# Performance work log

Hardware: AMD Instinct MI355X
Metric: run time of the kernel (lower is better)

The kernel has to match this reference:

```python
import jax, jax.numpy as jnp
import numpy as np

B, C, H, W = 16, 256, 32, 32
K = 3          # kernel size
KK = K * K     # matrix_batch = 9 kernel positions
N = 256        # out_channels = n (power of 2, nstack = 1)


def setup_inputs() -> dict:
    key = jax.random.key(0)
    k1, k2, k3, k4 = jax.random.split(key, 4)
    s = 1.0 / np.sqrt(2.0)  # repo's 'regular' param init scale
    return {
        "x": jax.random.normal(k1, (B, C, H, W), jnp.float32),
        "twiddle1": jax.random.normal(k2, (KK, N - 1, 2, 2), jnp.float32) * s,
        "twiddle2": jax.random.normal(k3, (KK, N - 1, 2, 2), jnp.float32) * s,
        "bias": jax.random.normal(k4, (KK, N), jnp.float32) * 0.01,
    }


def _butterfly_tied(twiddle, x, increasing):
    """Tied-weight butterfly multiply.
    twiddle: (s, n-1, 2, 2); x: (b, s, n). At stride st, twiddle[:, st-1:2*st-1]
    (length st) is shared across the n/(2*st) blocks (matches butterfly_mult_torch).
    """
    b, s, n = x.shape
    m = n.bit_length() - 1  # log2(n)
    strides = [1 << i for i in range(m)]
    if not increasing:
        strides = strides[::-1]
    for st in strides:
        t = twiddle[:, st - 1:2 * st - 1]            # (s, st, 2, 2)
        xr = x.reshape(b, s, n // (2 * st), 2, st)   # (b, s, g, 2, st)
        # out[b,s,g,i,l] = sum_k t[s,l,i,k] * xr[b,s,g,k,l]
        x = jnp.einsum('slik,bsgkl->bsgil', t, xr).reshape(b, s, n)
    return x


def reference(x, twiddle1, twiddle2, bias):
    b, c, h, w = x.shape
    # im2col / F.unfold with kernel 3, pad 1, stride 1 -> (b, c, 9, h*w),
    # kernel positions in row-major order (matches torch unfold layout).
    xp = jnp.pad(x, ((0, 0), (0, 0), (1, 1), (1, 1)))
    patches = jnp.stack(
        [xp[:, :, i:i + h, j:j + w] for i in range(K) for j in range(K)], axis=2
    )  # (b, c, 9, h, w)
    inp = patches.reshape(b, c, KK, h * w).transpose(0, 3, 2, 1)
    inp = inp.reshape(b * h * w, KK, c)  # (batch*h*w, 9, c)
    # BB^T: B^T (decreasing stride) then B (increasing stride), bias on last.
    y = _butterfly_tied(twiddle1, inp, increasing=False)
    y = _butterfly_tied(twiddle2, y, increasing=True) + bias  # bias: (9, N)
    out = y.mean(axis=1)  # average over the 9 kernel positions -> (b*h*w, N)
    return out.reshape(b, h * w, N).transpose(0, 2, 1).reshape(b, N, h, w)
```

## Files before the change

### kernel.cpp

```cpp
#include <hip/hip_runtime.h>
#include <hip/hip_bf16.h>

typedef __attribute__((ext_vector_type(8))) short short8;
typedef __attribute__((ext_vector_type(4))) float float4v;
typedef __attribute__((ext_vector_type(16))) float float16v;

#define XT_BYTES (16*32*34*34*8*2)
#define WG_BYTES (9*4*4*8*64*8*2)

__global__ __launch_bounds__(256) void k_prep(const float* __restrict__ x,
                                              const float* __restrict__ tw1,
                                              const float* __restrict__ tw2,
                                              const float* __restrict__ bias,
                                              __hip_bfloat16* __restrict__ xTg,
                                              __hip_bfloat16* __restrict__ Wg,
                                              float* __restrict__ biasout) {
  __shared__ __align__(16) char smem[256 * 33 * 4];
  int blk = blockIdx.x;
  int tid = threadIdx.x;

  if (blk < 512) {
    float* tile = (float*)smem;
    char* xTB = (char*)xTg;
    int h = blk & 31, b = blk >> 5;
    {
      int w4 = (tid & 7) * 4, c0 = tid >> 3;
#pragma unroll
      for (int j = 0; j < 8; ++j) {
        int ci = c0 + 32 * j;
        float4 v = *(const float4*)&x[((b * 256 + ci) * 32 + h) * 32 + w4];
        *(float4*)&tile[ci * 33 + w4] = v;
      }
    }
    __syncthreads();
    {
      int g0 = tid >> 5, w = tid & 31;
#pragma unroll
      for (int gi = 0; gi < 4; ++gi) {
        int g = gi * 8 + g0;
        union { short8 s; __hip_bfloat16 hv[8]; } pk;
#pragma unroll
        for (int cc = 0; cc < 8; ++cc)
          pk.hv[cc] = __float2bfloat16(tile[(g * 8 + cc) * 33 + w]);
        *(short8*)(xTB + ((((b * 32 + g) * 34 + h + 1) * 34) + (w + 1)) * 16) = pk.s;
      }
    }
    if (h < 2) {
      uint4 z4 = {0u, 0u, 0u, 0u};
      int edge = h * 33;
      for (int i = tid; i < 32 * 34; i += 256) {
        int g = i / 34, w = i - g * 34;
        *(uint4*)(xTB + ((((b * 32 + g) * 34 + edge) * 34) + w) * 16) = z4;
      }
      for (int i = tid; i < 32 * 32; i += 256) {
        int g = i >> 5, hh = 1 + (i & 31);
        *(uint4*)(xTB + ((((b * 32 + g) * 34 + hh) * 34) + edge) * 16) = z4;
      }
    }
    return;
  }

  int wblk = blk - 512;
  if (wblk == 144) {
    if (tid < 256) {
      float a = 0.f;
#pragma unroll
      for (int s = 0; s < 9; ++s) a += bias[s * 256 + tid];
      biasout[tid] = a * (1.f / 9.f);
    }
    return;
  }
  float* mat = (float*)smem;
  float* tws = (float*)(smem + 17408);
  int sidx = wblk >> 4;
  int colbase = (wblk & 15) * 16;

  for (int i = tid; i < 255 * 4; i += 256) {
    tws[i]           = tw1[sidx * 255 * 4 + i];
    tws[255 * 4 + i] = tw2[sidx * 255 * 4 + i];
  }
  {
    int r = tid;
#pragma unroll
    for (int c = 0; c < 16; ++c) mat[r * 17 + c] = (r == colbase + c) ? 1.f : 0.f;
  }

  int c  = tid & 15;
  int pg = tid >> 4;
  for (int ph = 0; ph < 2; ++ph) {
    for (int si = 0; si < 8; ++si) {
      int lg = ph ? si : (7 - si);
      int st = 1 << lg;
      __syncthreads();
      float x0[8], x1[8], t0[8], t1[8], t2[8], t3[8];
#pragma unroll
      for (int i = 0; i < 8; ++i) {
        int qp = pg * 8 + i;
        int li = qp & (st - 1);
        int gi = qp >> lg;
        int p0 = (gi << (lg + 1)) | li;
        int p1 = p0 + st;
        float4 tv = *(const float4*)&tws[(ph * 255 + st - 1 + li) * 4];
        t0[i] = tv.x; t1[i] = tv.y; t2[i] = tv.z; t3[i] = tv.w;
        x0[i] = mat[p0 * 17 + c];
        x1[i] = mat[p1 * 17 + c];
      }
#pragma unroll
      for (int i = 0; i < 8; ++i) {
        int qp = pg * 8 + i;
        int li = qp & (st - 1);
        int gi = qp >> lg;
        int p0 = (gi << (lg + 1)) | li;
        int p1 = p0 + st;
        mat[p0 * 17 + c] = t0[i] * x0[i] + t1[i] * x1[i];
        mat[p1 * 17 + c] = t2[i] * x0[i] + t3[i] * x1[i];
      }
    }
  }
  __syncthreads();

  for (int idx = tid; idx < 256 * 16; idx += 256) {
    int r = idx >> 4, cc = idx & 15;
    int cg = colbase + cc;
    int pr = cg >> 6, g = (cg >> 3) & 7, c8 = cg & 7;
    int nq = r >> 6, nl = r & 63;
    int o = ((((sidx * 4 + pr) * 4 + nq) * 8 + g) * 64 + nl) * 8 + c8;
    Wg[o] = __float2bfloat16(mat[r * 17 + cc] * (1.f / 9.f));
  }
}

__global__ __launch_bounds__(256, 4) void k_gemm(const __hip_bfloat16* __restrict__ xTg,
                                                 const __hip_bfloat16* __restrict__ Wg,
                                                 const float* __restrict__ biasout,
                                                 float* __restrict__ out) {
  __shared__ __align__(64) char lds[16384];
  const char* WgB = (const char*)Wg;
  const char* xTB = (const char*)xTg;

  int blk  = blockIdx.x;
  int rest = blk >> 3;
  int b    = 2 * (blk & 7) + (rest >> 6);
  int r2   = rest & 63;
  int nq   = r2 & 3;
  int pt   = r2 >> 2;
  int h0   = pt * 2;

  int tid  = threadIdx.x;
  int lane = tid & 63;
  int wk   = tid >> 6;
  int half = lane >> 5;
  int l31  = lane & 31;

  float16v acc[2][2];
#pragma unroll
  for (int mt = 0; mt < 2; ++mt)
#pragma unroll
    for (int p2 = 0; p2 < 2; ++p2)
#pragma unroll
      for (int e = 0; e < 16; ++e) acc[mt][p2][e] = 0.f;

  int aoff = ((2 * wk + half) * 64 + l31) * 16;
  int bbase = ((((b * 32 + 2 * wk + half) * 34 + h0) * 34) + l31) * 16;

#pragma unroll 2
  for (int p = 0; p < 4; ++p) {
    const char* Bp = xTB + bbase + p * (8 * 34 * 34) * 16;
    const char* Ap = WgB + (p * 4 + nq) * 8192;
#pragma unroll
    for (int si = 0; si < 3; ++si) {
#pragma unroll
      for (int sj = 0; sj < 3; ++sj) {
        const char* Aslab = Ap + (si * 3 + sj) * (16 * 8192);
        short8 a0 = *(const short8*)(Aslab + aoff);
        short8 a1 = *(const short8*)(Aslab + aoff + 32 * 16);
        const char* Bq = Bp + (si * 34 + sj) * 16;
        short8 b0 = *(const short8*)(Bq);
        short8 b1 = *(const short8*)(Bq + 34 * 16);
        acc[0][0] = __builtin_amdgcn_mfma_f32_32x32x16_bf16(a0, b0, acc[0][0], 0, 0, 0);
        acc[0][1] = __builtin_amdgcn_mfma_f32_32x32x16_bf16(a0, b1, acc[0][1], 0, 0, 0);
        acc[1][0] = __builtin_amdgcn_mfma_f32_32x32x16_bf16(a1, b0, acc[1][0], 0, 0, 0);
        acc[1][1] = __builtin_amdgcn_mfma_f32_32x32x16_bf16(a1, b1, acc[1][1], 0, 0, 0);
      }
    }
  }

  auto st16 = [&](int slot, const float16v& v) {
    char* base = lds + slot * 4096 + lane * 16;
    *(float4v*)(base)        = (float4v){v[0],  v[1],  v[2],  v[3]};
    *(float4v*)(base + 1024) = (float4v){v[4],  v[5],  v[6],  v[7]};
    *(float4v*)(base + 2048) = (float4v){v[8],  v[9],  v[10], v[11]};
    *(float4v*)(base + 3072) = (float4v){v[12], v[13], v[14], v[15]};
  };
  auto ld16add = [&](int slot, float16v& v) {
    const char* base = lds + slot * 4096 + lane * 16;
    float4v t0 = *(const float4v*)(base);
    float4v t1 = *(const float4v*)(base + 1024);
    float4v t2 = *(const float4v*)(base + 2048);
    float4v t3 = *(const float4v*)(base + 3072);
    v[0] += t0[0]; v[1] += t0[1]; v[2]  += t0[2]; v[3]  += t0[3];
    v[4] += t1[0]; v[5] += t1[1]; v[6]  += t1[2]; v[7]  += t1[3];
    v[8] += t2[0]; v[9] += t2[1]; v[10] += t2[2]; v[11] += t2[3];
    v[12] += t3[0]; v[13] += t3[1]; v[14] += t3[2]; v[15] += t3[3];
  };

  __syncthreads();
  if (wk >= 2) {
#pragma unroll
    for (int p2 = 0; p2 < 2; ++p2) st16((wk - 2) * 2 + p2, acc[0][p2]);
  }
  __syncthreads();
  if (wk < 2) {
#pragma unroll
    for (int p2 = 0; p2 < 2; ++p2) ld16add(wk * 2 + p2, acc[0][p2]);
  }
  __syncthreads();
  if (wk >= 2) {
#pragma unroll
    for (int p2 = 0; p2 < 2; ++p2) st16((wk - 2) * 2 + p2, acc[1][p2]);
  }
  __syncthreads();
  if (wk < 2) {
#pragma unroll
    for (int p2 = 0; p2 < 2; ++p2) ld16add(wk * 2 + p2, acc[1][p2]);
  }
  __syncthreads();
  if (wk == 1) {
#pragma unroll
    for (int p2 = 0; p2 < 2; ++p2) { st16(p2, acc[0][p2]); st16(2 + p2, acc[1][p2]); }
  }
  __syncthreads();
  if (wk == 0) {
#pragma unroll
    for (int p2 = 0; p2 < 2; ++p2) { ld16add(p2, acc[0][p2]); ld16add(2 + p2, acc[1][p2]); }
#pragma unroll
    for (int mt = 0; mt < 2; ++mt) {
#pragma unroll
      for (int reg = 0; reg < 16; ++reg) {
        int n = nq * 64 + mt * 32 + (reg & 3) + 8 * (reg >> 2) + 4 * half;
        float bv = biasout[n];
#pragma unroll
        for (int p2 = 0; p2 < 2; ++p2)
          out[((b * 256 + n) * 32 + h0 + p2) * 32 + l31] = acc[mt][p2][reg] + bv;
      }
    }
  }
}

extern "C" void kernel_launch(void* const* d_in, const int* in_sizes, int n_in,
                              void* d_out, int out_size, void* d_ws, size_t ws_size,
                              hipStream_t stream) {
  const float* x    = (const float*)d_in[0];
  const float* tw1  = (const float*)d_in[1];
  const float* tw2  = (const float*)d_in[2];
  const float* bias = (const float*)d_in[3];
  float* out = (float*)d_out;

  char* ws = (char*)d_ws;
  __hip_bfloat16* xTg = (__hip_bfloat16*)ws;
  __hip_bfloat16* Wg  = (__hip_bfloat16*)(ws + XT_BYTES);
  float* biasout      = (float*)(ws + XT_BYTES + WG_BYTES);

  k_prep<<<657, 256, 0, stream>>>(x, tw1, tw2, bias, xTg, Wg, biasout);
  k_gemm<<<1024, 256, 0, stream>>>(xTg, Wg, biasout, out);
}
```

Baseline: 108.4 us.

## Software-pipeline GEMM global loads with six-deep register ring and inline asm

Replaces the compiler-scheduled load/MFMA loop in k_gemm with a fully unrolled software pipeline. Loads of A and B fragments for six future steps are held in a register ring, issued via inline asm global_load_dwordx4 and gated by explicit s_waitcnt vmcnt counts, with sched barriers pinning the order. The aim is to hide global memory latency behind MFMA work. Occupancy hint drops from 4 to 2 blocks per SIMD to make room for the extra live registers, which may reduce latency hiding across waves.

```diff
diff --git a/kernel.cpp b/kernel.cpp
--- a/kernel.cpp
+++ b/kernel.cpp
@@ -129,7 +129,30 @@
   }
 }
 
-__global__ __launch_bounds__(256, 4) void k_gemm(const __hip_bfloat16* __restrict__ xTg,
+
+#define ISSUE(SL, P, S, SI, SJ)                                               \
+  { const char* ap_ = pA + (P)*32768 + (S)*131072;                            \
+    const char* bp_ = pB + (P)*147968 + (SI)*544 + (SJ)*16;                   \
+    asm volatile("global_load_dwordx4 %0, %2, off\n\t"                        \
+                 "global_load_dwordx4 %1, %2, off offset:512"                 \
+      : "=&v"(ra[SL][0]), "=&v"(ra[SL][1]) : "v"(ap_));                       \
+    asm volatile("global_load_dwordx4 %0, %2, off\n\t"                        \
+                 "global_load_dwordx4 %1, %2, off offset:544"                 \
+      : "=&v"(rb[SL][0]), "=&v"(rb[SL][1]) : "v"(bp_)); }
+
+#define WAITB_(N) asm volatile("s_waitcnt vmcnt(" #N ")" ::: "memory")
+#define WAITB(N) WAITB_(N); __builtin_amdgcn_sched_barrier(0)
+
+#define MM4(SL)                                                               \
+  acc[0][0] = __builtin_amdgcn_mfma_f32_32x32x16_bf16(ra[SL][0], rb[SL][0], acc[0][0], 0, 0, 0); \
+  acc[0][1] = __builtin_amdgcn_mfma_f32_32x32x16_bf16(ra[SL][0], rb[SL][1], acc[0][1], 0, 0, 0); \
+  acc[1][0] = __builtin_amdgcn_mfma_f32_32x32x16_bf16(ra[SL][1], rb[SL][0], acc[1][0], 0, 0, 0); \
+  acc[1][1] = __builtin_amdgcn_mfma_f32_32x32x16_bf16(ra[SL][1], rb[SL][1], acc[1][1], 0, 0, 0);
+
+#define BODY(SL, JP, JS, JSI, JSJ) { WAITB(20); MM4(SL); ISSUE(SL, JP, JS, JSI, JSJ); }
+#define BODYT(SL, N)               { WAITB(N);  MM4(SL); }
+
+__global__ __launch_bounds__(256, 2) void k_gemm(const __hip_bfloat16* __restrict__ xTg,
                                                  const __hip_bfloat16* __restrict__ Wg,
                                                  const float* __restrict__ biasout,
                                                  float* __restrict__ out) {
@@ -160,29 +183,27 @@
       for (int e = 0; e < 16; ++e) acc[mt][p2][e] = 0.f;
 
   int aoff = ((2 * wk + half) * 64 + l31) * 16;
+  const char* pA = WgB + nq * 8192 + aoff;
   int bbase = ((((b * 32 + 2 * wk + half) * 34 + h0) * 34) + l31) * 16;
-
-#pragma unroll 2
-  for (int p = 0; p < 4; ++p) {
-    const char* Bp = xTB + bbase + p * (8 * 34 * 34) * 16;
-    const char* Ap = WgB + (p * 4 + nq) * 8192;
-#pragma unroll
-    for (int si = 0; si < 3; ++si) {
-#pragma unroll
-      for (int sj = 0; sj < 3; ++sj) {
-        const char* Aslab = Ap + (si * 3 + sj) * (16 * 8192);
-        short8 a0 = *(const short8*)(Aslab + aoff);
-        short8 a1 = *(const short8*)(Aslab + aoff + 32 * 16);
-        const char* Bq = Bp + (si * 34 + sj) * 16;
-        short8 b0 = *(const short8*)(Bq);
-        short8 b1 = *(const short8*)(Bq + 34 * 16);
-        acc[0][0] = __builtin_amdgcn_mfma_f32_32x32x16_bf16(a0, b0, acc[0][0], 0, 0, 0);
-        acc[0][1] = __builtin_amdgcn_mfma_f32_32x32x16_bf16(a0, b1, acc[0][1], 0, 0, 0);
-        acc[1][0] = __builtin_amdgcn_mfma_f32_32x32x16_bf16(a1, b0, acc[1][0], 0, 0, 0);
-        acc[1][1] = __builtin_amdgcn_mfma_f32_32x32x16_bf16(a1, b1, acc[1][1], 0, 0, 0);
-      }
-    }
-  }
+  const char* pB = xTB + bbase;
+
+  short8 ra[6][2];
+  short8 rb[6][2];
+
+  ISSUE(0, 0,0,0,0) ISSUE(1, 0,1,0,1) ISSUE(2, 0,2,0,2)
+  ISSUE(3, 0,3,1,0) ISSUE(4, 0,4,1,1) ISSUE(5, 0,5,1,2)
+
+  BODY(0, 0,6,2,0) BODY(1, 0,7,2,1) BODY(2, 0,8,2,2)
+  BODY(3, 1,0,0,0) BODY(4, 1,1,0,1) BODY(5, 1,2,0,2)
+  BODY(0, 1,3,1,0) BODY(1, 1,4,1,1) BODY(2, 1,5,1,2)
+  BODY(3, 1,6,2,0) BODY(4, 1,7,2,1) BODY(5, 1,8,2,2)
+  BODY(0, 2,0,0,0) BODY(1, 2,1,0,1) BODY(2, 2,2,0,2)
+  BODY(3, 2,3,1,0) BODY(4, 2,4,1,1) BODY(5, 2,5,1,2)
+  BODY(0, 2,6,2,0) BODY(1, 2,7,2,1) BODY(2, 2,8,2,2)
+  BODY(3, 3,0,0,0) BODY(4, 3,1,0,1) BODY(5, 3,2,0,2)
+  BODY(0, 3,3,1,0) BODY(1, 3,4,1,1) BODY(2, 3,5,1,2)
+  BODY(3, 3,6,2,0) BODY(4, 3,7,2,1) BODY(5, 3,8,2,2)
+  BODYT(0, 20) BODYT(1, 16) BODYT(2, 12) BODYT(3, 8) BODYT(4, 4) BODYT(5, 0)
 
   auto st16 = [&](int slot, const float16v& v) {
     char* base = lds + slot * 4096 + lane * 16;
```

Measured after the change: 109.5 us. No clear change (+1.0%).
